# Performance work log

Hardware: AMD Instinct MI355X
Metric: run time of the kernel (lower is better)

The kernel has to match this reference:

```python
import math
import jax, jax.numpy as jnp
import numpy as np

B, NPC, K, D, T, L = 512, 32, 12, 64, 64, 4  # crystals, atoms/crystal, knn, node_dim, time_dim, layers
N = B * NPC
E_IN = 2 * D + 1 + T   # 193
N_IN = 2 * D + T       # 192


def setup_inputs() -> dict:
    key = jax.random.key(0)
    ks = jax.random.split(key, 32)
    rn = lambda k, shp, s=0.05: jax.random.normal(k, shp, jnp.float32) * s
    inp = {}
    inp["z_nodes"] = jax.random.normal(ks[0], (N, 128), jnp.float32)
    inp["t"] = jax.random.uniform(ks[1], (B,), jnp.float32) * 1000.0
    inp["frac_coords"] = jax.random.uniform(ks[2], (N, 3), jnp.float32)
    inp["lattice"] = jnp.eye(3, dtype=jnp.float32) * 5.0 + rn(ks[3], (B, 3, 3), 0.3)
    inp["batch_indices"] = jnp.repeat(jnp.arange(B, dtype=jnp.int32), NPC)
    inp["num_atoms"] = NPC
    # time_mlp: Linear(T, 2T) -> SiLU -> Linear(2T, T)
    inp["time_w1"] = rn(ks[4], (T, 2 * T)); inp["time_b1"] = rn(ks[5], (2 * T,))
    inp["time_w2"] = rn(ks[6], (2 * T, T)); inp["time_b2"] = rn(ks[7], (T,))
    # node_embedding: Linear(128, D)
    inp["emb_w"] = rn(ks[8], (128, D)); inp["emb_b"] = rn(ks[9], (D,))
    # per-layer EGNN params stacked on leading L axis
    inp["edge_w1"] = rn(ks[10], (L, E_IN, D)); inp["edge_b1"] = rn(ks[11], (L, D))
    inp["edge_w2"] = rn(ks[12], (L, D, D));    inp["edge_b2"] = rn(ks[13], (L, D))
    inp["coord_w1"] = rn(ks[14], (L, D, D));   inp["coord_b1"] = rn(ks[15], (L, D))
    inp["coord_w2"] = rn(ks[16], (L, D, 1))
    inp["node_w1"] = rn(ks[17], (L, N_IN, D)); inp["node_b1"] = rn(ks[18], (L, D))
    inp["node_w2"] = rn(ks[19], (L, D, D));    inp["node_b2"] = rn(ks[20], (L, D))
    return inp


def _forward(z_nodes, t, frac_coords, lattice, batch_indices, num_atoms,
             time_w1, time_b1, time_w2, time_b2, emb_w, emb_b,
             edge_w1, edge_b1, edge_w2, edge_b2, coord_w1, coord_b1, coord_w2,
             node_w1, node_b1, node_w2, node_b2):
    silu = jax.nn.silu
    n = num_atoms
    b = lattice.shape[0]
    n_nodes = z_nodes.shape[0]

    # ---- time embedding ----
    half = T // 2
    freqs = jnp.exp(jnp.arange(half, dtype=jnp.float32) * (-math.log(10000.0) / (half - 1)))
    ang = t[:, None] * freqs[None, :]
    sinu = jnp.concatenate([jnp.sin(ang), jnp.cos(ang)], axis=-1)  # [B, T]
    t_feat = silu(sinu @ time_w1 + time_b1) @ time_w2 + time_b2     # [B, T]
    t_nodes = t_feat[batch_indices]                                  # [N, T]

    h = z_nodes @ emb_w + emb_b                                      # [N, D]

    # ---- vectorized PBC KNN graph (all crystals have n atoms) ----
    f = frac_coords.reshape(b, n, 3)
    diff_f = f[:, :, None, :] - f[:, None, :, :]
    diff_f = diff_f - jnp.round(diff_f)
    diff_c = jnp.einsum('bijk,bkl->bijl', diff_f, lattice)           # [b,n,n,3]
    dist_sq = jnp.sum(diff_c * diff_c, axis=-1)                      # [b,n,n]
    dist_sq = jnp.where(jnp.eye(n, dtype=bool)[None], jnp.inf, dist_sq)
    k = min(K, n - 1)
    _, idx = jax.lax.top_k(-dist_sq, k)                              # [b,n,k] neighbor indices
    offs = (jnp.arange(b, dtype=jnp.int32) * n)[:, None, None]
    edge_src = (idx + offs).reshape(-1)                              # neighbors j
    edge_dst = (jnp.broadcast_to(jnp.arange(n, dtype=jnp.int32)[None, :, None], (b, n, k)) + offs).reshape(-1)
    diff_cart = jnp.take_along_axis(diff_c, jnp.broadcast_to(idx[..., None], (b, n, k, 3)), axis=2).reshape(-1, 3)
    dist_sq_e = jnp.take_along_axis(dist_sq, idx, axis=2).reshape(-1, 1)

    t_edges = t_nodes[edge_src]                                      # [E, T]

    total_shift = jnp.zeros((n_nodes, 3), dtype=h.dtype)
    for l in range(L):
        edge_in = jnp.concatenate([h[edge_src], h[edge_dst], dist_sq_e, t_edges], axis=-1)
        m = silu(edge_in @ edge_w1[l] + edge_b1[l])
        m = silu(m @ edge_w2[l] + edge_b2[l])                        # [E, D]
        cw = silu(m @ coord_w1[l] + coord_b1[l]) @ coord_w2[l]       # [E, 1]
        coord_update = jax.ops.segment_sum(diff_cart * cw, edge_src, num_segments=n_nodes)
        m_i = jax.ops.segment_sum(m, edge_dst, num_segments=n_nodes)
        node_in = jnp.concatenate([h, m_i, t_nodes], axis=-1)
        h = h + (silu(node_in @ node_w1[l] + node_b1[l]) @ node_w2[l] + node_b2[l])
        total_shift = total_shift + coord_update

    inv_lat = jnp.linalg.inv(lattice)[batch_indices]                 # [N,3,3]
    shift_frac = jnp.einsum('ni,nij->nj', total_shift, inv_lat)
    return shift_frac, h


def reference(z_nodes, t, frac_coords, lattice, batch_indices, num_atoms,
              time_w1, time_b1, time_w2, time_b2, emb_w, emb_b,
              edge_w1, edge_b1, edge_w2, edge_b2, coord_w1, coord_b1, coord_w2,
              node_w1, node_b1, node_w2, node_b2):
    return _forward(z_nodes, t, frac_coords, lattice, batch_indices, num_atoms,
                    time_w1, time_b1, time_w2, time_b2, emb_w, emb_b,
                    edge_w1, edge_b1, edge_w2, edge_b2, coord_w1, coord_b1, coord_w2,
                    node_w1, node_b1, node_w2, node_b2)
```

## Files before the change

### kernel.cpp

```cpp
#include <hip/hip_runtime.h>
#include <hip/hip_bf16.h>
#include <math.h>

#define NB 512
#define NPC 32
#define KNN 12
#define NL 4
#define NN (NB*NPC)
#define WPL 28672
#define TSTR 68

typedef float v4f __attribute__((ext_vector_type(4)));
typedef float v2f __attribute__((ext_vector_type(2)));
typedef short s8v __attribute__((ext_vector_type(8)));

__device__ __forceinline__ float silu_f(float x) {
    return x * __builtin_amdgcn_rcpf(1.0f + __builtin_amdgcn_exp2f(x * -1.44269504088896341f));
}

__device__ __forceinline__ v2f silu2(v2f x) {
    v2f n = x * -1.44269504088896341f;
    v2f e; e.x = __builtin_amdgcn_exp2f(n.x); e.y = __builtin_amdgcn_exp2f(n.y);
    v2f d = e + 1.0f;
    v2f r; r.x = __builtin_amdgcn_rcpf(d.x); r.y = __builtin_amdgcn_rcpf(d.y);
    return x * r;
}

__device__ __forceinline__ unsigned short f2bf(float x) {
    unsigned u = __float_as_uint(x);
    u += 0x7fffu + ((u >> 16) & 1u);
    return (unsigned short)(u >> 16);
}

__device__ __forceinline__ unsigned pk2bf(float a, float b) {
    __hip_bfloat162 t = __float22bfloat162_rn(make_float2(a, b));
    union { __hip_bfloat162 h; unsigned u; } c; c.h = t;
    return c.u;
}
__device__ __forceinline__ unsigned pk2bfu(v2f s) { return pk2bf(s.x, s.y); }

__device__ __forceinline__ int div12(int e) { return (e * 1366) >> 14; }

template<int R>
__device__ __forceinline__ void gemm_acc(const float* A, int astride,
                                         const float* __restrict__ Wg,
                                         int K, int lane, float* acc) {
#pragma unroll 2
    for (int kq = 0; kq < (K >> 2); ++kq) {
        float w0 = Wg[(4*kq+0)*64 + lane];
        float w1 = Wg[(4*kq+1)*64 + lane];
        float w2 = Wg[(4*kq+2)*64 + lane];
        float w3 = Wg[(4*kq+3)*64 + lane];
#pragma unroll
        for (int r = 0; r < R; ++r) {
            float4 a = *(const float4*)(A + r*astride + 4*kq);
            acc[r] = fmaf(a.x, w0, acc[r]);
            acc[r] = fmaf(a.y, w1, acc[r]);
            acc[r] = fmaf(a.z, w2, acc[r]);
            acc[r] = fmaf(a.w, w3, acc[r]);
        }
    }
}

extern "C" __global__ void prepack_w(const float* __restrict__ edge_w1, const float* __restrict__ edge_w2,
                                     const float* __restrict__ coord_w1, const float* __restrict__ node_w1,
                                     const float* __restrict__ node_w2, unsigned short* __restrict__ wout) {
    int g = blockIdx.x * 256 + threadIdx.x;
    if (g >= 4 * WPL / 8) return;
    int l = (g * 8) / WPL;
    int r = (g * 8) % WPL;
    int base, nKt, mat;
    if      (r < 8192)  { base = 0;     nKt = 2; mat = 0; }
    else if (r < 12288) { base = 8192;  nKt = 2; mat = 1; }
    else if (r < 16384) { base = 12288; nKt = 2; mat = 2; }
    else if (r < 24576) { base = 16384; nKt = 4; mat = 3; }
    else                { base = 24576; nKt = 2; mat = 4; }
    int idx = r - base;
    int lane = (idx >> 3) & 63, t = idx >> 9;
    int kt = t % nKt, nt = t / nKt;
    int k0 = kt*32 + ((lane >> 4) & 3)*8;
    int n  = nt*16 + (lane & 15);
    unsigned short o[8];
#pragma unroll
    for (int j = 0; j < 8; ++j) {
        int k = k0 + j;
        float v;
        if      (mat == 0) v = (n < 64) ? edge_w1[l*193*64 + k*64 + n] : edge_w1[l*193*64 + (64+k)*64 + (n-64)];
        else if (mat == 1) v = edge_w2 [l*4096 + k*64 + n];
        else if (mat == 2) v = coord_w1[l*4096 + k*64 + n];
        else if (mat == 3) v = node_w1 [l*192*64 + k*64 + n];
        else               v = node_w2 [l*4096 + k*64 + n];
        o[j] = f2bf(v);
    }
    *(s8v*)(wout + g*8) = *(s8v*)o;
}

extern "C" __global__ __launch_bounds__(512, 2)
void crystal_fused(const float* __restrict__ z_nodes, const float* __restrict__ t_in,
                   const float* __restrict__ frac,    const float* __restrict__ lattice,
                   const float* __restrict__ time_w1, const float* __restrict__ time_b1,
                   const float* __restrict__ time_w2, const float* __restrict__ time_b2,
                   const float* __restrict__ emb_w,   const float* __restrict__ emb_b,
                   const float* __restrict__ edge_w1, const float* __restrict__ edge_b1,
                   const float* __restrict__ edge_b2, const float* __restrict__ coord_b1,
                   const float* __restrict__ coord_w2,
                   const float* __restrict__ node_w1, const float* __restrict__ node_b1,
                   const float* __restrict__ node_b2,
                   const unsigned short* __restrict__ wbf,
                   float* __restrict__ out)
{
    __shared__ __align__(16) float s_h[32*65];
    __shared__ __align__(16) unsigned short s_habf[32*136];
    __shared__ __align__(16) float s_hs[32*68];
    __shared__ __align__(16) float s_hd[32*68];
    __shared__ __align__(16) unsigned short s_tiles16[8*16*TSTR];
    __shared__ __align__(16) unsigned short s_w2bf[4096];
    __shared__ float2 s_emeta[384];
    __shared__ float s_endc[384*3];
    __shared__ float s_frac[32][3];
    __shared__ float s_lat[9], s_inv[9];
    __shared__ float s_sinu[64], s_t1[128], s_tf[64];
    __shared__ float s_tb4[NL*64], s_nb4[NL*64];
    __shared__ float s_shift[32*3];

    float* dcf = (float*)s_tiles16;
    float (*s_dsq)[33] = (float(*)[33])((char*)s_tiles16 + 12288);
    unsigned short* s_n1bf = s_tiles16;

    const int tid  = threadIdx.x;
    const int c    = blockIdx.x;
    const int lane = tid & 63;
    const int wave = tid >> 6;
    const int q4   = lane >> 4;
    const int c16  = lane & 15;
    const int base = c * NPC;

    if (tid < 96) {
        ((float*)s_frac)[tid] = frac[base*3 + tid];
    } else if (tid < 105) {
        s_lat[tid-96] = lattice[c*9 + (tid-96)];
    } else if (tid >= 128 && tid < 160) {
        int i = tid - 128;
        float freq = expf((float)i * (-9.210340371976184f / 31.0f));
        float ang  = t_in[c] * freq;
        s_sinu[i]    = sinf(ang);
        s_sinu[i+32] = cosf(ang);
    }
    __syncthreads();

    {
        float l00=s_lat[0],l01=s_lat[1],l02=s_lat[2];
        float l10=s_lat[3],l11=s_lat[4],l12=s_lat[5];
        float l20=s_lat[6],l21=s_lat[7],l22=s_lat[8];
        for (int p = tid; p < 1024; p += 512) {
            int i = p >> 5, j = p & 31;
            float dx = s_frac[i][0]-s_frac[j][0];
            float dy = s_frac[i][1]-s_frac[j][1];
            float dz = s_frac[i][2]-s_frac[j][2];
            dx -= rintf(dx); dy -= rintf(dy); dz -= rintf(dz);
            float cx = dx*l00 + dy*l10 + dz*l20;
            float cy = dx*l01 + dy*l11 + dz*l21;
            float cz = dx*l02 + dy*l12 + dz*l22;
            float dd = cx*cx + cy*cy + cz*cz;
            s_dsq[i][j] = (i==j) ? 3.0e38f : dd;
            dcf[p*3+0]=cx; dcf[p*3+1]=cy; dcf[p*3+2]=cz;
        }
    }
    __syncthreads();

    if (tid < 256) {
        int i = tid >> 3, g = tid & 7;
        float d0 = s_dsq[i][g*4+0];
        float d1 = s_dsq[i][g*4+1];
        float d2 = s_dsq[i][g*4+2];
        float d3 = s_dsq[i][g*4+3];
        for (int k = 0; k < KNN; ++k) {
            float v = d0; int jl = g*4;
            if (d1 < v) { v = d1; jl = g*4+1; }
            if (d2 < v) { v = d2; jl = g*4+2; }
            if (d3 < v) { v = d3; jl = g*4+3; }
            float ov; int oj;
            ov = __shfl_xor(v, 1); oj = __shfl_xor(jl, 1);
            if (ov < v || (ov == v && oj < jl)) { v = ov; jl = oj; }
            ov = __shfl_xor(v, 2); oj = __shfl_xor(jl, 2);
            if (ov < v || (ov == v && oj < jl)) { v = ov; jl = oj; }
            ov = __shfl_xor(v, 4); oj = __shfl_xor(jl, 4);
            if (ov < v || (ov == v && oj < jl)) { v = ov; jl = oj; }
            if ((jl >> 2) == g) {
                int s = jl & 3;
                if      (s == 0) d0 = 3.9e38f;
                else if (s == 1) d1 = 3.9e38f;
                else if (s == 2) d2 = 3.9e38f;
                else             d3 = 3.9e38f;
            }
            if (g == 0) {
                int e = i*KNN + k;
                s_emeta[e] = make_float2(v, __int_as_float(jl));
                int p = (i<<5) + jl;
                s_endc[e*3+0] = dcf[p*3+0];
                s_endc[e*3+1] = dcf[p*3+1];
                s_endc[e*3+2] = dcf[p*3+2];
            }
        }
    } else if (tid < 384) {
        int jj = tid - 256;
        float p0 = time_b1[jj], p1=0.f, p2=0.f, p3=0.f;
        for (int k = 0; k < 64; k += 4) {
            p0 = fmaf(s_sinu[k+0], time_w1[(k+0)*128+jj], p0);
            p1 = fmaf(s_sinu[k+1], time_w1[(k+1)*128+jj], p1);
            p2 = fmaf(s_sinu[k+2], time_w1[(k+2)*128+jj], p2);
            p3 = fmaf(s_sinu[k+3], time_w1[(k+3)*128+jj], p3);
        }
        s_t1[jj] = silu_f((p0+p1) + (p2+p3));
    }
    __syncthreads();

    if (tid < 64) {
        float p0=time_b2[tid],p1=0.f,p2=0.f,p3=0.f;
        for (int k = 0; k < 128; k += 4) {
            p0 = fmaf(s_t1[k+0], time_w2[(k+0)*64+tid], p0);
            p1 = fmaf(s_t1[k+1], time_w2[(k+1)*64+tid], p1);
            p2 = fmaf(s_t1[k+2], time_w2[(k+2)*64+tid], p2);
            p3 = fmaf(s_t1[k+3], time_w2[(k+3)*64+tid], p3);
        }
        s_tf[tid] = (p0+p1) + (p2+p3);
    } else if (tid < 160) {
        s_shift[tid-64] = 0.0f;
    }
    __syncthreads();

    {
        int lt = wave >> 1, kind = wave & 1;
        const float* Wt = kind ? (node_w1 + lt*192*64 + 128*64) : (edge_w1 + lt*193*64 + 129*64);
        const float* bb = kind ? (node_b1 + lt*64) : (edge_b1 + lt*64);
        float p0 = bb[lane], p1=0.f, p2=0.f, p3=0.f;
        for (int k = 0; k < 64; k += 4) {
            p0 = fmaf(s_tf[k+0], Wt[(k+0)*64 + lane], p0);
            p1 = fmaf(s_tf[k+1], Wt[(k+1)*64 + lane], p1);
            p2 = fmaf(s_tf[k+2], Wt[(k+2)*64 + lane], p2);
            p3 = fmaf(s_tf[k+3], Wt[(k+3)*64 + lane], p3);
        }
        float v = (p0+p1) + (p2+p3);
        if (kind) s_nb4[lt*64 + lane] = v;
        else      s_tb4[lt*64 + lane] = v;
    }
    {
        float acc[4];
#pragma unroll
        for (int r = 0; r < 4; ++r) acc[r] = emb_b[lane];
        gemm_acc<4>(z_nodes + (base + wave*4)*128, 128, emb_w, 128, lane, acc);
#pragma unroll
        for (int r = 0; r < 4; ++r) {
            int row = wave*4 + r;
            s_h[row*65 + lane] = acc[r];
            s_habf[row*136 + lane] = f2bf(acc[r]);
        }
    }
    __syncthreads();

    for (int l = 0; l < NL; ++l) {
        const unsigned short* wl = wbf + l*WPL;
        const float* w1row = edge_w1 + l*193*64 + 128*64;

        *(s8v*)(s_w2bf + tid*8) = *(const s8v*)(wl + 8192 + tid*8);

        float b2e_v[4], cb1_v[4], w2c_v[4];
#pragma unroll
        for (int nt = 0; nt < 4; ++nt) {
            b2e_v[nt] = edge_b2 [l*64 + nt*16 + c16];
            cb1_v[nt] = coord_b1[l*64 + nt*16 + c16];
            w2c_v[nt] = coord_w2[l*64 + nt*16 + c16];
        }

        s8v wc1f[8];
#pragma unroll
        for (int nt = 0; nt < 4; ++nt)
#pragma unroll
            for (int kt = 0; kt < 2; ++kt)
                wc1f[nt*2+kt] = *(const s8v*)(wl + 12288 + ((nt*2+kt)*64 + lane)*8);
        union F4 { float4 v; float f[4]; };
        F4 W4[4];
        W4[0].v = *(const float4*)(w1row + q4*8);
        W4[1].v = *(const float4*)(w1row + q4*8 + 4);
        W4[2].v = *(const float4*)(w1row + 32 + q4*8);
        W4[3].v = *(const float4*)(w1row + 32 + q4*8 + 4);

        {
            const int wn = wave & 3;
            s8v a[2][2];
#pragma unroll
            for (int mt = 0; mt < 2; ++mt)
#pragma unroll
                for (int kt = 0; kt < 2; ++kt)
                    a[mt][kt] = *(const s8v*)(s_habf + (mt*16 + c16)*136 + kt*32 + q4*8);
            v4f acc[2] = {{0.f,0.f,0.f,0.f},{0.f,0.f,0.f,0.f}};
#pragma unroll
            for (int kt = 0; kt < 2; ++kt) {
                s8v b = *(const s8v*)(wl + (((wn + (wave >= 4 ? 4 : 0))*2 + kt)*64 + lane)*8);
#pragma unroll
                for (int mt = 0; mt < 2; ++mt)
                    acc[mt] = __builtin_amdgcn_mfma_f32_16x16x32_bf16(a[mt][kt], b, acc[mt], 0, 0, 0);
            }
            int col = wn*16 + c16;
            if (wave >= 4) {
                float tbv = s_tb4[l*64 + col];
#pragma unroll
                for (int mt = 0; mt < 2; ++mt)
#pragma unroll
                    for (int reg = 0; reg < 4; ++reg)
                        s_hd[(mt*16 + q4*4 + reg)*68 + col] = acc[mt][reg] + tbv;
            } else {
#pragma unroll
                for (int mt = 0; mt < 2; ++mt)
#pragma unroll
                    for (int reg = 0; reg < 4; ++reg)
                        s_hs[(mt*16 + q4*4 + reg)*68 + col] = acc[mt][reg];
            }
        }
        __syncthreads();

        {
            unsigned short* tile = s_tiles16 + wave*16*TSTR;
            float miacc[4][2];
#pragma unroll
            for (int a2 = 0; a2 < 4; ++a2) { miacc[a2][0] = 0.f; miacc[a2][1] = 0.f; }

            auto flushd = [&](int d) {
                int s = d & 1;
#pragma unroll
                for (int nt = 0; nt < 4; ++nt) {
                    float v = miacc[nt][s];
                    v += __shfl_xor(v, 16);
                    v += __shfl_xor(v, 32);
                    s_habf[(wave*4 + d)*136 + 64 + nt*16 + c16] = f2bf(v);
                    miacc[nt][s] = 0.f;
                }
            };

            float2 me0 = s_emeta[wave*48 +  0 + c16];
            float2 me1 = s_emeta[wave*48 + 16 + c16];
            float2 me2 = s_emeta[wave*48 + 32 + c16];

#pragma unroll
            for (int m = 0; m < 3; ++m) {
                const int e0g = wave*48 + m*16;
                const float2 me = (m==0) ? me0 : (m==1) ? me1 : me2;
                const float dq = me.x;
                F4 H[4], G[4];
                {
                    int srcn = __float_as_int(me.y);
                    int dstn = div12(e0g + c16);
                    const float* hsr = s_hs + srcn*68 + q4*8;
                    const float* hdr = s_hd + dstn*68 + q4*8;
                    H[0].v = *(const float4*)(hsr);      H[1].v = *(const float4*)(hsr+4);
                    H[2].v = *(const float4*)(hsr+32);   H[3].v = *(const float4*)(hsr+36);
                    G[0].v = *(const float4*)(hdr);      G[1].v = *(const float4*)(hdr+4);
                    G[2].v = *(const float4*)(hdr+32);   G[3].v = *(const float4*)(hdr+36);
                }
                union S8 { s8v v; unsigned u[4]; } A0, A1;
#pragma unroll
                for (int g2 = 0; g2 < 4; ++g2) {
                    v2f h0 = {H[g2].f[0], H[g2].f[1]}, h1 = {H[g2].f[2], H[g2].f[3]};
                    v2f g0 = {G[g2].f[0], G[g2].f[1]}, g1 = {G[g2].f[2], G[g2].f[3]};
                    v2f w0 = {W4[g2].f[0], W4[g2].f[1]}, w1 = {W4[g2].f[2], W4[g2].f[3]};
                    v2f t0 = h0 + g0 + w0 * dq;
                    v2f t1 = h1 + g1 + w1 * dq;
                    unsigned lo  = pk2bfu(silu2(t0));
                    unsigned hi2 = pk2bfu(silu2(t1));
                    if (g2 < 2) { A0.u[g2*2] = lo; A0.u[g2*2+1] = hi2; }
                    else        { A1.u[(g2-2)*2] = lo; A1.u[(g2-2)*2+1] = hi2; }
                }

                const int thr = 3 - m;
                const int slo = m & 1;
#pragma unroll
                for (int nt = 0; nt < 4; ++nt) {
                    s8v b0 = *(const s8v*)(s_w2bf + ((nt*2+0)*64 + lane)*8);
                    s8v b1 = *(const s8v*)(s_w2bf + ((nt*2+1)*64 + lane)*8);
                    v4f acc = {0.f,0.f,0.f,0.f};
                    acc = __builtin_amdgcn_mfma_f32_16x16x32_bf16(A0.v, b0, acc, 0,0,0);
                    acc = __builtin_amdgcn_mfma_f32_16x16x32_bf16(A1.v, b1, acc, 0,0,0);
                    int col = nt*16 + c16;
                    v2f z01 = {acc[0] + b2e_v[nt], acc[1] + b2e_v[nt]};
                    v2f z23 = {acc[2] + b2e_v[nt], acc[3] + b2e_v[nt]};
                    v2f s01 = silu2(z01), s23 = silu2(z23);
                    unsigned p01 = pk2bfu(s01), p23 = pk2bfu(s23);
                    tile[(q4*4 + 0)*TSTR + col] = (unsigned short)p01;
                    tile[(q4*4 + 1)*TSTR + col] = (unsigned short)(p01 >> 16);
                    tile[(q4*4 + 2)*TSTR + col] = (unsigned short)p23;
                    tile[(q4*4 + 3)*TSTR + col] = (unsigned short)(p23 >> 16);
                    float msum = (s01.x + s01.y) + (s23.x + s23.y);
                    bool hi = (q4 >= thr);
                    miacc[nt][slo]     += hi ? 0.f : msum;
                    miacc[nt][slo ^ 1] += hi ? msum : 0.f;
                }
                asm volatile("s_waitcnt lgkmcnt(0)" ::: "memory");
                s8v c0 = *(const s8v*)(tile + c16*TSTR +      q4*8);
                s8v c1 = *(const s8v*)(tile + c16*TSTR + 32 + q4*8);
                v2f cwp01 = {0.f, 0.f}, cwp23 = {0.f, 0.f};
#pragma unroll
                for (int nt = 0; nt < 4; ++nt) {
                    v4f acc = {0.f,0.f,0.f,0.f};
                    acc = __builtin_amdgcn_mfma_f32_16x16x32_bf16(c0, wc1f[nt*2+0], acc, 0,0,0);
                    acc = __builtin_amdgcn_mfma_f32_16x16x32_bf16(c1, wc1f[nt*2+1], acc, 0,0,0);
                    v2f z01 = {acc[0] + cb1_v[nt], acc[1] + cb1_v[nt]};
                    v2f z23 = {acc[2] + cb1_v[nt], acc[3] + cb1_v[nt]};
                    cwp01 += silu2(z01) * w2c_v[nt];
                    cwp23 += silu2(z23) * w2c_v[nt];
                }
                float cwp[4] = {cwp01.x, cwp01.y, cwp23.x, cwp23.y};
#pragma unroll
                for (int reg = 0; reg < 4; ++reg) {
                    float v = cwp[reg];
                    v += __shfl_xor(v, 1); v += __shfl_xor(v, 2);
                    v += __shfl_xor(v, 4); v += __shfl_xor(v, 8);
                    int e = e0g + q4*4 + reg;
                    if (c16 < 3) {
                        int src = __float_as_int(s_emeta[e].y);
                        atomicAdd(&s_shift[src*3 + c16], s_endc[e*3 + c16] * v);
                    }
                }
                if (m == 0)      { flushd(0); }
                else if (m == 1) { flushd(1); }
                else             { flushd(2); flushd(3); }
            }
        }

        const int mtA = wave & 1, ntA = wave >> 1;
        s8v bn1[4];
#pragma unroll
        for (int kt = 0; kt < 4; ++kt)
            bn1[kt] = *(const s8v*)(wl + 16384 + ((ntA*4+kt)*64 + lane)*8);
        __syncthreads();

        {
            s8v aA[4];
#pragma unroll
            for (int kt = 0; kt < 4; ++kt)
                aA[kt] = *(const s8v*)(s_habf + (mtA*16 + c16)*136 + kt*32 + q4*8);
            int col = ntA*16 + c16;
            float nbc = s_nb4[l*64 + col];
            v4f acc = {0.f,0.f,0.f,0.f};
#pragma unroll
            for (int kt = 0; kt < 4; ++kt)
                acc = __builtin_amdgcn_mfma_f32_16x16x32_bf16(aA[kt], bn1[kt], acc, 0,0,0);
            v2f z01 = {acc[0] + nbc, acc[1] + nbc};
            v2f z23 = {acc[2] + nbc, acc[3] + nbc};
            unsigned p01 = pk2bfu(silu2(z01)), p23 = pk2bfu(silu2(z23));
            int r0 = mtA*16 + q4*4;
            s_n1bf[(r0+0)*72 + col] = (unsigned short)p01;
            s_n1bf[(r0+1)*72 + col] = (unsigned short)(p01 >> 16);
            s_n1bf[(r0+2)*72 + col] = (unsigned short)p23;
            s_n1bf[(r0+3)*72 + col] = (unsigned short)(p23 >> 16);
        }
        s8v bn2[2];
        bn2[0] = *(const s8v*)(wl + 24576 + ((ntA*2+0)*64 + lane)*8);
        bn2[1] = *(const s8v*)(wl + 24576 + ((ntA*2+1)*64 + lane)*8);
        __syncthreads();

        {
            s8v a0 = *(const s8v*)(s_n1bf + (mtA*16 + c16)*72 +      q4*8);
            s8v a1 = *(const s8v*)(s_n1bf + (mtA*16 + c16)*72 + 32 + q4*8);
            int col = ntA*16 + c16;
            float nb2_v = node_b2[l*64 + col];
            v4f acc = {0.f,0.f,0.f,0.f};
            acc = __builtin_amdgcn_mfma_f32_16x16x32_bf16(a0, bn2[0], acc, 0,0,0);
            acc = __builtin_amdgcn_mfma_f32_16x16x32_bf16(a1, bn2[1], acc, 0,0,0);
#pragma unroll
            for (int reg = 0; reg < 4; ++reg) {
                int row = mtA*16 + q4*4 + reg;
                float hn = s_h[row*65 + col] + acc[reg] + nb2_v;
                s_h[row*65 + col] = hn;
                s_habf[row*136 + col] = f2bf(hn);
            }
        }
        __syncthreads();
    }

    if (tid == 0) {
        float a=s_lat[0],b=s_lat[1],cc=s_lat[2];
        float d=s_lat[3],e=s_lat[4],f =s_lat[5];
        float g=s_lat[6],h2=s_lat[7],i2=s_lat[8];
        float A  =  (e*i2 - f*h2);
        float Bm = -(d*i2 - f*g);
        float C  =  (d*h2 - e*g);
        float det = a*A + b*Bm + cc*C;
        float rd = 1.0f/det;
        s_inv[0] = A*rd;
        s_inv[1] = -(b*i2 - cc*h2)*rd;
        s_inv[2] =  (b*f  - cc*e )*rd;
        s_inv[3] = Bm*rd;
        s_inv[4] =  (a*i2 - cc*g )*rd;
        s_inv[5] = -(a*f  - cc*d )*rd;
        s_inv[6] = C*rd;
        s_inv[7] = -(a*h2 - b*g  )*rd;
        s_inv[8] =  (a*e  - b*d  )*rd;
    }
    __syncthreads();
    if (tid < 96) {
        int r = tid/3, j = tid%3;
        float v = s_shift[r*3+0]*s_inv[0*3+j]
                + s_shift[r*3+1]*s_inv[1*3+j]
                + s_shift[r*3+2]*s_inv[2*3+j];
        out[(base + r)*3 + j] = v;
    }
    for (int q = tid; q < 2048; q += 512) {
        int row = q >> 6, colq = q & 63;
        out[NN*3 + base*64 + q] = s_h[row*65 + colq];
    }
}

extern "C" void kernel_launch(void* const* d_in, const int* in_sizes, int n_in,
                              void* d_out, int out_size, void* d_ws, size_t ws_size,
                              hipStream_t stream) {
    unsigned short* wbf = (unsigned short*)d_ws;
    prepack_w<<<(4*WPL/8 + 255)/256, 256, 0, stream>>>(
        (const float*)d_in[12], (const float*)d_in[14], (const float*)d_in[16],
        (const float*)d_in[19], (const float*)d_in[21], wbf);
    crystal_fused<<<NB, 512, 0, stream>>>(
        (const float*)d_in[0],  (const float*)d_in[1],  (const float*)d_in[2],  (const float*)d_in[3],
        (const float*)d_in[6],  (const float*)d_in[7],  (const float*)d_in[8],  (const float*)d_in[9],
        (const float*)d_in[10], (const float*)d_in[11],
        (const float*)d_in[12], (const float*)d_in[13], (const float*)d_in[15],
        (const float*)d_in[17], (const float*)d_in[18],
        (const float*)d_in[19], (const float*)d_in[20], (const float*)d_in[22],
        wbf, (float*)d_out);
}
```

Measured before the change: 229.6 us.

## Raise occupancy target by moving weights to LDS and node state to registers

```diff
diff --git a/kernel.cpp b/kernel.cpp
--- a/kernel.cpp
+++ b/kernel.cpp
@@ -95,7 +95,7 @@
     *(s8v*)(wout + g*8) = *(s8v*)o;
 }
 
-extern "C" __global__ __launch_bounds__(512, 2)
+extern "C" __global__ __launch_bounds__(512, 4)
 void crystal_fused(const float* __restrict__ z_nodes, const float* __restrict__ t_in,
                    const float* __restrict__ frac,    const float* __restrict__ lattice,
                    const float* __restrict__ time_w1, const float* __restrict__ time_b1,
@@ -109,13 +109,15 @@
                    const unsigned short* __restrict__ wbf,
                    float* __restrict__ out)
 {
-    __shared__ __align__(16) float s_h[32*65];
     __shared__ __align__(16) unsigned short s_habf[32*136];
     __shared__ __align__(16) float s_hs[32*68];
     __shared__ __align__(16) float s_hd[32*68];
     __shared__ __align__(16) unsigned short s_tiles16[8*16*TSTR];
     __shared__ __align__(16) unsigned short s_w2bf[4096];
-    __shared__ float2 s_emeta[384];
+    __shared__ __align__(16) unsigned short s_wc1bf[4096];
+    __shared__ __align__(16) float s_w1r[64];
+    __shared__ float s_edsq[384];
+    __shared__ unsigned short s_esrc[384];
     __shared__ float s_endc[384*3];
     __shared__ float s_frac[32][3];
     __shared__ float s_lat[9], s_inv[9];
@@ -125,6 +127,7 @@
 
     float* dcf = (float*)s_tiles16;
     float (*s_dsq)[33] = (float(*)[33])((char*)s_tiles16 + 12288);
+    float* s_hf = (float*)s_tiles16;
     unsigned short* s_n1bf = s_tiles16;
 
     const int tid  = threadIdx.x;
@@ -195,7 +198,8 @@
             }
             if (g == 0) {
                 int e = i*KNN + k;
-                s_emeta[e] = make_float2(v, __int_as_float(jl));
+                s_edsq[e] = v;
+                s_esrc[e] = (unsigned short)jl;
                 int p = (i<<5) + jl;
                 s_endc[e*3+0] = dcf[p*3+0];
                 s_endc[e*3+1] = dcf[p*3+1];
@@ -252,17 +256,27 @@
 #pragma unroll
         for (int r = 0; r < 4; ++r) {
             int row = wave*4 + r;
-            s_h[row*65 + lane] = acc[r];
+            s_hf[row*64 + lane] = acc[r];
             s_habf[row*136 + lane] = f2bf(acc[r]);
         }
     }
     __syncthreads();
+
+    const int mtA = wave & 1, ntA = wave >> 1;
+    float h_reg[4];
+    {
+        int colh = ntA*16 + c16;
+#pragma unroll
+        for (int r = 0; r < 4; ++r)
+            h_reg[r] = s_hf[(mtA*16 + q4*4 + r)*64 + colh];
+    }
 
     for (int l = 0; l < NL; ++l) {
         const unsigned short* wl = wbf + l*WPL;
-        const float* w1row = edge_w1 + l*193*64 + 128*64;
-
-        *(s8v*)(s_w2bf + tid*8) = *(const s8v*)(wl + 8192 + tid*8);
+
+        *(s8v*)(s_w2bf  + tid*8) = *(const s8v*)(wl +  8192 + tid*8);
+        *(s8v*)(s_wc1bf + tid*8) = *(const s8v*)(wl + 12288 + tid*8);
+        if (tid < 64) s_w1r[tid] = edge_w1[l*193*64 + 128*64 + tid];
 
         float b2e_v[4], cb1_v[4], w2c_v[4];
 #pragma unroll
@@ -271,19 +285,6 @@
             cb1_v[nt] = coord_b1[l*64 + nt*16 + c16];
             w2c_v[nt] = coord_w2[l*64 + nt*16 + c16];
         }
-
-        s8v wc1f[8];
-#pragma unroll
-        for (int nt = 0; nt < 4; ++nt)
-#pragma unroll
-            for (int kt = 0; kt < 2; ++kt)
-                wc1f[nt*2+kt] = *(const s8v*)(wl + 12288 + ((nt*2+kt)*64 + lane)*8);
-        union F4 { float4 v; float f[4]; };
-        F4 W4[4];
-        W4[0].v = *(const float4*)(w1row + q4*8);
-        W4[1].v = *(const float4*)(w1row + q4*8 + 4);
-        W4[2].v = *(const float4*)(w1row + 32 + q4*8);
-        W4[3].v = *(const float4*)(w1row + 32 + q4*8 + 4);
 
         {
             const int wn = wave & 3;
@@ -337,34 +338,23 @@
                 }
             };
 
-            float2 me0 = s_emeta[wave*48 +  0 + c16];
-            float2 me1 = s_emeta[wave*48 + 16 + c16];
-            float2 me2 = s_emeta[wave*48 + 32 + c16];
-
-#pragma unroll
+#pragma unroll 1
             for (int m = 0; m < 3; ++m) {
                 const int e0g = wave*48 + m*16;
-                const float2 me = (m==0) ? me0 : (m==1) ? me1 : me2;
-                const float dq = me.x;
-                F4 H[4], G[4];
-                {
-                    int srcn = __float_as_int(me.y);
-                    int dstn = div12(e0g + c16);
-                    const float* hsr = s_hs + srcn*68 + q4*8;
-                    const float* hdr = s_hd + dstn*68 + q4*8;
-                    H[0].v = *(const float4*)(hsr);      H[1].v = *(const float4*)(hsr+4);
-                    H[2].v = *(const float4*)(hsr+32);   H[3].v = *(const float4*)(hsr+36);
-                    G[0].v = *(const float4*)(hdr);      G[1].v = *(const float4*)(hdr+4);
-                    G[2].v = *(const float4*)(hdr+32);   G[3].v = *(const float4*)(hdr+36);
-                }
+                const float dq = s_edsq[e0g + c16];
+                const int srcn = s_esrc[e0g + c16];
+                const int dstn = div12(e0g + c16);
+                const float* hsr = s_hs + srcn*68;
+                const float* hdr = s_hd + dstn*68;
                 union S8 { s8v v; unsigned u[4]; } A0, A1;
 #pragma unroll
                 for (int g2 = 0; g2 < 4; ++g2) {
-                    v2f h0 = {H[g2].f[0], H[g2].f[1]}, h1 = {H[g2].f[2], H[g2].f[3]};
-                    v2f g0 = {G[g2].f[0], G[g2].f[1]}, g1 = {G[g2].f[2], G[g2].f[3]};
-                    v2f w0 = {W4[g2].f[0], W4[g2].f[1]}, w1 = {W4[g2].f[2], W4[g2].f[3]};
-                    v2f t0 = h0 + g0 + w0 * dq;
-                    v2f t1 = h1 + g1 + w1 * dq;
+                    int off = ((g2 & 2) ? 32 : 0) + ((g2 & 1) ? 4 : 0) + q4*8;
+                    float4 Hv = *(const float4*)(hsr + off);
+                    float4 Gv = *(const float4*)(hdr + off);
+                    float4 Wv = *(const float4*)(s_w1r + off);
+                    v2f t0 = {Hv.x + Gv.x + Wv.x*dq, Hv.y + Gv.y + Wv.y*dq};
+                    v2f t1 = {Hv.z + Gv.z + Wv.z*dq, Hv.w + Gv.w + Wv.w*dq};
                     unsigned lo  = pk2bfu(silu2(t0));
                     unsigned hi2 = pk2bfu(silu2(t1));
                     if (g2 < 2) { A0.u[g2*2] = lo; A0.u[g2*2+1] = hi2; }
@@ -400,9 +390,11 @@
                 v2f cwp01 = {0.f, 0.f}, cwp23 = {0.f, 0.f};
 #pragma unroll
                 for (int nt = 0; nt < 4; ++nt) {
+                    s8v wb0 = *(const s8v*)(s_wc1bf + ((nt*2+0)*64 + lane)*8);
+                    s8v wb1 = *(const s8v*)(s_wc1bf + ((nt*2+1)*64 + lane)*8);
                     v4f acc = {0.f,0.f,0.f,0.f};
-                    acc = __builtin_amdgcn_mfma_f32_16x16x32_bf16(c0, wc1f[nt*2+0], acc, 0,0,0);
-                    acc = __builtin_amdgcn_mfma_f32_16x16x32_bf16(c1, wc1f[nt*2+1], acc, 0,0,0);
+                    acc = __builtin_amdgcn_mfma_f32_16x16x32_bf16(c0, wb0, acc, 0,0,0);
+                    acc = __builtin_amdgcn_mfma_f32_16x16x32_bf16(c1, wb1, acc, 0,0,0);
                     v2f z01 = {acc[0] + cb1_v[nt], acc[1] + cb1_v[nt]};
                     v2f z23 = {acc[2] + cb1_v[nt], acc[3] + cb1_v[nt]};
                     cwp01 += silu2(z01) * w2c_v[nt];
@@ -416,7 +408,7 @@
                     v += __shfl_xor(v, 4); v += __shfl_xor(v, 8);
                     int e = e0g + q4*4 + reg;
                     if (c16 < 3) {
-                        int src = __float_as_int(s_emeta[e].y);
+                        int src = s_esrc[e];
                         atomicAdd(&s_shift[src*3 + c16], s_endc[e*3 + c16] * v);
                     }
                 }
@@ -426,7 +418,6 @@
             }
         }
 
-        const int mtA = wave & 1, ntA = wave >> 1;
         s8v bn1[4];
 #pragma unroll
         for (int kt = 0; kt < 4; ++kt)
@@ -469,9 +460,10 @@
 #pragma unroll
             for (int reg = 0; reg < 4; ++reg) {
                 int row = mtA*16 + q4*4 + reg;
-                float hn = s_h[row*65 + col] + acc[reg] + nb2_v;
-                s_h[row*65 + col] = hn;
-                s_habf[row*136 + col] = f2bf(hn);
+                float hn = h_reg[reg] + acc[reg] + nb2_v;
+                h_reg[reg] = hn;
+                if (l < NL-1) s_habf[row*136 + col] = f2bf(hn);
+                else          out[NN*3 + base*64 + row*64 + col] = hn;
             }
         }
         __syncthreads();
@@ -504,10 +496,6 @@
                 + s_shift[r*3+2]*s_inv[2*3+j];
         out[(base + r)*3 + j] = v;
     }
-    for (int q = tid; q < 2048; q += 512) {
-        int row = q >> 6, colq = q & 63;
-        out[NN*3 + base*64 + q] = s_h[row*65 + colq];
-    }
 }
 
 extern "C" void kernel_launch(void* const* d_in, const int* in_sizes, int n_in,
```

New measurement: 211.8 us. 1.08x faster.
